# Optimization experiments

Hardware: AMD Instinct MI355X
Metric: run time of the kernel (lower is better)

## Reference

```python
import jax, jax.numpy as jnp
import numpy as np

IN_CH = 32
OUT_CH = 32
HIDDEN = 32  # edge/angle MLP hidden width


def setup_inputs() -> dict:
    key = jax.random.key(0)
    ks = jax.random.split(key, 13)
    N, E, A = 50000, 200000, 400000
    s = 0.1
    return {
        "x": jax.random.normal(ks[0], (N, IN_CH), dtype=jnp.float32),
        "edge_index": jax.random.randint(ks[1], (2, E), 0, N),
        "edge_attr": jax.random.uniform(ks[2], (E, 1), dtype=jnp.float32),
        "angle_index": jax.random.randint(ks[3], (3, A), 0, N),
        "angles": jax.random.uniform(ks[4], (A, 1), dtype=jnp.float32),
        # edge_mlp: Linear(1,32) -> ReLU -> Linear(32, in*out)
        "eW1": jax.random.normal(ks[5], (1, HIDDEN), dtype=jnp.float32) * s,
        "eb1": jax.random.normal(ks[6], (HIDDEN,), dtype=jnp.float32) * s,
        "eW2": jax.random.normal(ks[7], (HIDDEN, IN_CH * OUT_CH), dtype=jnp.float32) * s,
        "eb2": jax.random.normal(ks[8], (IN_CH * OUT_CH,), dtype=jnp.float32) * s,
        # angle_mlp: Linear(1,32) -> ReLU -> Linear(32, out)
        "aW1": jax.random.normal(ks[9], (1, HIDDEN), dtype=jnp.float32) * s,
        "ab1": jax.random.normal(ks[10], (HIDDEN,), dtype=jnp.float32) * s,
        "aW2": jax.random.normal(ks[11], (HIDDEN, OUT_CH), dtype=jnp.float32) * s,
        "ab2": jax.random.normal(ks[12], (OUT_CH,), dtype=jnp.float32) * s,
    }


def reference(x, edge_index, edge_attr, angle_index, angles,
              eW1, eb1, eW2, eb2, aW1, ab1, aW2, ab2):
    N = x.shape[0]
    row, col = edge_index[0], edge_index[1]
    # per-edge weight matrices from edge MLP: (E, in, out)
    h = jax.nn.relu(edge_attr @ eW1 + eb1)
    edge_w = (h @ eW2 + eb2).reshape(-1, IN_CH, OUT_CH)
    # gather source node features, apply per-edge matrix (bmm)
    msg = jnp.einsum('ei,eio->eo', x[col], edge_w)  # (E, out)
    agg = jax.ops.segment_sum(msg, row, num_segments=N)
    # angle branch: scatter angle features onto center node j
    j = angle_index[1]
    angle_feat = jax.nn.relu(angles @ aW1 + ab1) @ aW2 + ab2  # (A, out)
    agg = agg + jax.ops.segment_sum(angle_feat, j, num_segments=N)
    return agg
```

## Files before the change

### kernel.cpp

```cpp
#include <hip/hip_runtime.h>
#include <hip/hip_bf16.h>
#include <stdint.h>

#define IC 32
#define OC 32
#define HID 32

#define PBIN 16
#define TSH 44
#define TSCALE 1048576.0f

typedef __attribute__((ext_vector_type(8))) _Float16 half8;
typedef __attribute__((ext_vector_type(4))) float f32x4;
typedef unsigned long long u64;

static __device__ __forceinline__ _Float16 f2h(float f) { return (_Float16)f; }

__global__ void zero_kernel(float* __restrict__ out, int n) {
    int i = (blockIdx.x * blockDim.x + threadIdx.x) * 4;
    if (i + 3 < n) {
        *(float4*)(out + i) = make_float4(0.f, 0.f, 0.f, 0.f);
    } else {
        for (int k = i; k < n; ++k) out[k] = 0.f;
    }
}

__global__ __launch_bounds__(256) void angle_scatter(
    const float* __restrict__ angles, const int* __restrict__ angle_index,
    const float* __restrict__ aW1, const float* __restrict__ ab1,
    u64* __restrict__ cells, int A)
{
    float w1[HID], b1[HID];
#pragma unroll
    for (int k = 0; k < HID; ++k) { w1[k] = aW1[k]; b1[k] = ab1[k]; }

    int i0 = blockIdx.x * blockDim.x + threadIdx.x;
    int stride = gridDim.x * blockDim.x;
    for (int a = i0; a < A; a += stride) {
        const float t = angles[a];
        const int j = angle_index[A + a];
        int c = 0, c0 = 0;
#pragma unroll
        for (int k = 0; k < HID; ++k) {
            const bool pos = w1[k] > 0.f;
            const bool on  = fmaf(t, w1[k], b1[k]) > 0.f;
            const bool on0 = b1[k] > 0.f;
            c  += (pos ? on  : !on ) ? 1 : 0;
            c0 += (pos ? on0 : !on0) ? 1 : 0;
        }
        const int cc = c - c0;
        if ((unsigned)cc < (unsigned)PBIN) {
            const u64 enc = ((u64)1 << TSH) | (u64)(unsigned)(t * TSCALE);
            atomicAdd(cells + (size_t)j * PBIN + cc, enc);
        }
    }
}

__global__ __launch_bounds__(256) void angle_gather(
    float* __restrict__ out,
    const float* __restrict__ aW1, const float* __restrict__ ab1,
    const float* __restrict__ aW2, const float* __restrict__ ab2,
    int N)
{
    const int lane = threadIdx.x & 63;
    const int o    = lane & 31;
    const int half = lane >> 5;
    const int wib  = threadIdx.x >> 6;
    const int gw   = blockIdx.x * (blockDim.x >> 6) + wib;
    const int nodesPerIter = gridDim.x * (blockDim.x >> 6) * 2;

    float w1[HID], b1[HID], w2[HID];
#pragma unroll
    for (int k = 0; k < HID; ++k) {
        w1[k] = aW1[k];
        b1[k] = ab1[k];
        w2[k] = aW2[k * OC + o];
    }
    const float bias = ab2[o];

    for (int j = gw * 2 + half; j < N; j += nodesPerIter) {
        const u64* cj = (const u64*)out + (size_t)j * PBIN;
        float acc = 0.f, tot = 0.f;
#pragma unroll
        for (int cc = 0; cc < PBIN; ++cc) {
            const u64 v = cj[cc];
            if (v) {
                const float n  = (float)(unsigned)(v >> TSH);
                const float ts = (float)(v & (((u64)1 << TSH) - 1)) * (1.f / TSCALE);
                const float tb = ts / n;
                float s = 0.f;
#pragma unroll
                for (int k = 0; k < HID; ++k) {
                    float h = fmaf(tb, w1[k], b1[k]);
                    h = h > 0.f ? h : 0.f;
                    s = fmaf(h, w2[k], s);
                }
                acc = fmaf(n, s, acc);
                tot += n;
            }
        }
        out[(size_t)j * OC + o] = fmaf(tot, bias, acc);
    }
}

__global__ __launch_bounds__(256) void angle_fixup(
    const float* __restrict__ angles, const int* __restrict__ angle_index,
    const float* __restrict__ aW1, const float* __restrict__ ab1,
    const float* __restrict__ aW2, const float* __restrict__ ab2,
    float* __restrict__ out, int A)
{
    float w1[HID], b1[HID];
#pragma unroll
    for (int k = 0; k < HID; ++k) { w1[k] = aW1[k]; b1[k] = ab1[k]; }

    int c0 = 0, c1 = 0;
#pragma unroll
    for (int k = 0; k < HID; ++k) {
        const bool pos = w1[k] > 0.f;
        const bool f0 = pos ? (b1[k] > 0.f) : !(b1[k] > 0.f);
        const bool f1 = pos ? ((w1[k] + b1[k]) > 0.f) : !((w1[k] + b1[k]) > 0.f);
        c0 += f0 ? 1 : 0;
        c1 += f1 ? 1 : 0;
    }
    if (c1 - c0 + 1 <= PBIN) return;

    int i0 = blockIdx.x * blockDim.x + threadIdx.x;
    int stride = gridDim.x * blockDim.x;
    for (int a = i0; a < A; a += stride) {
        const float t = angles[a];
        const int j = angle_index[A + a];
        int c = 0;
#pragma unroll
        for (int k = 0; k < HID; ++k) {
            const bool pos = w1[k] > 0.f;
            const bool on  = fmaf(t, w1[k], b1[k]) > 0.f;
            c += (pos ? on : !on) ? 1 : 0;
        }
        if (c - c0 >= PBIN) {
            float h[HID];
#pragma unroll
            for (int k = 0; k < HID; ++k) {
                float v = fmaf(t, w1[k], b1[k]);
                h[k] = v > 0.f ? v : 0.f;
            }
            for (int o = 0; o < OC; ++o) {
                float s = ab2[o];
#pragma unroll
                for (int k = 0; k < HID; ++k) s = fmaf(h[k], aW2[k * OC + o], s);
                unsafeAtomicAdd(out + (size_t)j * OC + o, s);
            }
        }
    }
}

__global__ __launch_bounds__(256) void edge_kernel(
    const float* __restrict__ x, const int* __restrict__ edge_index,
    const float* __restrict__ edge_attr,
    const float* __restrict__ eW1, const float* __restrict__ eb1,
    const float* __restrict__ eW2, const float* __restrict__ eb2,
    float* __restrict__ out, int E)
{
    const int tid   = threadIdx.x;
    const int lane  = tid & 63;
    const int gwave = blockIdx.x * 4 + (tid >> 6);
    const int ot    = gwave & 1;
    const int tile0 = gwave >> 1;
    const int tstride = (gridDim.x * 4) >> 1;
    const int q     = lane >> 4;
    const int l15   = lane & 15;
    const int ocol  = ot * 16 + l15;

    half8 Bf[33];
#pragma unroll
    for (int s = 0; s < 32; ++s) {
        half8 b;
#pragma unroll
        for (int j = 0; j < 8; ++j)
            b[j] = f2h(eW2[s * 1024 + (q * 8 + j) * 32 + ocol]);
        Bf[s] = b;
    }
    {
        half8 b;
#pragma unroll
        for (int j = 0; j < 8; ++j)
            b[j] = f2h(eb2[(q * 8 + j) * 32 + ocol]);
        Bf[32] = b;
    }

    const int numTiles = (E + 15) >> 4;

    for (int tile = tile0; tile < numTiles; tile += 2 * tstride) {
        const int tA = tile;
        const int tB = tile + tstride;
        const bool hasB = (tB < numTiles);

        const int eA  = (tA << 4) + l15;
        const bool va = (eA < E);
        const int eAc = va ? eA : 0;
        const float ta = va ? edge_attr[eAc] : 0.f;
        const int colA = va ? edge_index[E + eAc] : 0;

        const int eB  = (tB << 4) + l15;
        const bool vb = hasB && (eB < E);
        const int eBc = vb ? eB : 0;
        const float tb = vb ? edge_attr[eBc] : 0.f;
        const int colB = vb ? edge_index[E + eBc] : 0;

        const float* xpA = x + (size_t)colA * IC + q * 8;
        const float4 xloA = *(const float4*)(xpA);
        const float4 xhiA = *(const float4*)(xpA + 4);
        const float* xpB = x + (size_t)colB * IC + q * 8;
        const float4 xloB = *(const float4*)(xpB);
        const float4 xhiB = *(const float4*)(xpB + 4);

        int dstsA[4], dstsB[4];
        const int ebaseA = (tA << 4) + q * 4;
        const int ebaseB = (tB << 4) + q * 4;
#pragma unroll
        for (int r = 0; r < 4; ++r) {
            const int erA = ebaseA + r;
            dstsA[r] = (erA < E) ? edge_index[erA] : -1;
            const int erB = ebaseB + r;
            dstsB[r] = (hasB && erB < E) ? edge_index[erB] : -1;
        }

        half8 xhA, xhB;
        xhA[0] = f2h(xloA.x); xhA[1] = f2h(xloA.y);
        xhA[2] = f2h(xloA.z); xhA[3] = f2h(xloA.w);
        xhA[4] = f2h(xhiA.x); xhA[5] = f2h(xhiA.y);
        xhA[6] = f2h(xhiA.z); xhA[7] = f2h(xhiA.w);
        xhB[0] = f2h(xloB.x); xhB[1] = f2h(xloB.y);
        xhB[2] = f2h(xloB.z); xhB[3] = f2h(xloB.w);
        xhB[4] = f2h(xhiB.x); xhB[5] = f2h(xhiB.y);
        xhB[6] = f2h(xhiB.z); xhB[7] = f2h(xhiB.w);

        f32x4 accA = {0.f, 0.f, 0.f, 0.f};
        f32x4 accB = {0.f, 0.f, 0.f, 0.f};
#pragma unroll
        for (int s = 0; s < 32; ++s) {
            const float w1s = eW1[s], b1s = eb1[s];
            float hsA = fmaf(ta, w1s, b1s);
            hsA = hsA > 0.f ? hsA : 0.f;
            float hsB = fmaf(tb, w1s, b1s);
            hsB = hsB > 0.f ? hsB : 0.f;
            const _Float16 hA = f2h(hsA);
            const _Float16 hB = f2h(hsB);
            half8 hvA = {hA, hA, hA, hA, hA, hA, hA, hA};
            half8 hvB = {hB, hB, hB, hB, hB, hB, hB, hB};
            half8 aA = xhA * hvA;
            half8 aB = xhB * hvB;
            accA = __builtin_amdgcn_mfma_f32_16x16x32_f16(aA, Bf[s], accA, 0, 0, 0);
            accB = __builtin_amdgcn_mfma_f32_16x16x32_f16(aB, Bf[s], accB, 0, 0, 0);
        }
        {
            accA = __builtin_amdgcn_mfma_f32_16x16x32_f16(xhA, Bf[32], accA, 0, 0, 0);
            accB = __builtin_amdgcn_mfma_f32_16x16x32_f16(xhB, Bf[32], accB, 0, 0, 0);
        }

#pragma unroll
        for (int r = 0; r < 4; ++r) {
            if (dstsA[r] >= 0)
                unsafeAtomicAdd(out + (size_t)dstsA[r] * OC + ocol, accA[r]);
        }
#pragma unroll
        for (int r = 0; r < 4; ++r) {
            if (dstsB[r] >= 0)
                unsafeAtomicAdd(out + (size_t)dstsB[r] * OC + ocol, accB[r]);
        }
    }
}

extern "C" void kernel_launch(void* const* d_in, const int* in_sizes, int n_in,
                              void* d_out, int out_size, void* d_ws, size_t ws_size,
                              hipStream_t stream)
{
    const float* x          = (const float*)d_in[0];
    const int*   edge_index = (const int*)d_in[1];
    const float* edge_attr  = (const float*)d_in[2];
    const int*   angle_index= (const int*)d_in[3];
    const float* angles     = (const float*)d_in[4];
    const float* eW1        = (const float*)d_in[5];
    const float* eb1        = (const float*)d_in[6];
    const float* eW2        = (const float*)d_in[7];
    const float* eb2        = (const float*)d_in[8];
    const float* aW1        = (const float*)d_in[9];
    const float* ab1        = (const float*)d_in[10];
    const float* aW2        = (const float*)d_in[11];
    const float* ab2        = (const float*)d_in[12];
    float* out = (float*)d_out;
    (void)d_ws; (void)ws_size;

    const int E = in_sizes[1] / 2;
    const int A = in_sizes[3] / 3;
    const int N = in_sizes[0] / IC;

    const int zblocks = (out_size / 4 + 255) / 256;
    zero_kernel<<<zblocks, 256, 0, stream>>>(out, out_size);

    const int sblocks = (A + 255) / 256;
    angle_scatter<<<sblocks, 256, 0, stream>>>(angles, angle_index,
                                               aW1, ab1, (u64*)out, A);

    const int gblocks = (N + 7) / 8;
    angle_gather<<<gblocks, 256, 0, stream>>>(out, aW1, ab1, aW2, ab2, N);

    angle_fixup<<<sblocks, 256, 0, stream>>>(angles, angle_index,
                                             aW1, ab1, aW2, ab2, out, A);

    edge_kernel<<<512, 256, 0, stream>>>(x, edge_index, edge_attr,
                                         eW1, eb1, eW2, eb2, out, E);
}
```

Measured before the change: 191.9 us.

## Rewrite angle_gather to accumulate hidden activations and apply aW2 via MFMA

The angle gather kernel now sums per-cell hidden activations, weighted by cell count, for 16 nodes per wave, with each quarter-wave handling 8 of the 32 hidden units. It then applies the second layer with two fp16 16x16x32 MFMA instructions instead of a per-output scalar dot product for every cell. It also limits the loop over cells to the number of possible ReLU pieces computed from the weights, rather than always walking all 16 bins. This removes most of the redundant scalar FMAs and bin reads, but rounds the accumulated activations and aW2 to fp16, which may cost accuracy.

```diff
diff --git a/kernel.cpp b/kernel.cpp
--- a/kernel.cpp
+++ b/kernel.cpp
@@ -63,43 +63,73 @@
     int N)
 {
     const int lane = threadIdx.x & 63;
-    const int o    = lane & 31;
-    const int half = lane >> 5;
+    const int q    = lane >> 4;
+    const int l15  = lane & 15;
     const int wib  = threadIdx.x >> 6;
-    const int gw   = blockIdx.x * (blockDim.x >> 6) + wib;
-    const int nodesPerIter = gridDim.x * (blockDim.x >> 6) * 2;
-
-    float w1[HID], b1[HID], w2[HID];
+    const int base = (blockIdx.x * 4 + wib) * 16;
+    if (base >= N) return;
+
+    float w1s[8], b1s[8];
+    int c0 = 0, c1 = 0;
 #pragma unroll
     for (int k = 0; k < HID; ++k) {
-        w1[k] = aW1[k];
-        b1[k] = ab1[k];
-        w2[k] = aW2[k * OC + o];
-    }
-    const float bias = ab2[o];
-
-    for (int j = gw * 2 + half; j < N; j += nodesPerIter) {
-        const u64* cj = (const u64*)out + (size_t)j * PBIN;
-        float acc = 0.f, tot = 0.f;
-#pragma unroll
-        for (int cc = 0; cc < PBIN; ++cc) {
-            const u64 v = cj[cc];
-            if (v) {
-                const float n  = (float)(unsigned)(v >> TSH);
-                const float ts = (float)(v & (((u64)1 << TSH) - 1)) * (1.f / TSCALE);
-                const float tb = ts / n;
-                float s = 0.f;
-#pragma unroll
-                for (int k = 0; k < HID; ++k) {
-                    float h = fmaf(tb, w1[k], b1[k]);
-                    h = h > 0.f ? h : 0.f;
-                    s = fmaf(h, w2[k], s);
-                }
-                acc = fmaf(n, s, acc);
-                tot += n;
+        const float w = aW1[k], b = ab1[k];
+        const bool pos = w > 0.f;
+        const bool f0 = pos ? (b > 0.f) : !(b > 0.f);
+        const bool f1 = pos ? ((w + b) > 0.f) : !((w + b) > 0.f);
+        c0 += f0 ? 1 : 0;
+        c1 += f1 ? 1 : 0;
+        if ((k >> 3) == q) { w1s[k & 7] = w; b1s[k & 7] = b; }
+    }
+    int npc = c1 - c0 + 1;
+    if (npc > PBIN) npc = PBIN;
+
+    half8 Bf0, Bf1;
+#pragma unroll
+    for (int j = 0; j < 8; ++j) {
+        Bf0[j] = f2h(aW2[(q * 8 + j) * OC + l15]);
+        Bf1[j] = f2h(aW2[(q * 8 + j) * OC + 16 + l15]);
+    }
+    const float bias0 = ab2[l15];
+    const float bias1 = ab2[16 + l15];
+
+    const int jn = base + l15;
+    const bool vn = (jn < N);
+    const u64* cj = (const u64*)out + (size_t)(vn ? jn : 0) * PBIN;
+    float g[8] = {0.f, 0.f, 0.f, 0.f, 0.f, 0.f, 0.f, 0.f};
+    float tot = 0.f;
+    for (int cc = 0; cc < npc; ++cc) {
+        const u64 v = vn ? cj[cc] : 0;
+        if (v) {
+            const float n  = (float)(unsigned)(v >> TSH);
+            const float ts = (float)(v & (((u64)1 << TSH) - 1)) * (1.f / TSCALE);
+            const float tb = ts / n;
+#pragma unroll
+            for (int k = 0; k < 8; ++k) {
+                float h = fmaf(tb, w1s[k], b1s[k]);
+                h = h > 0.f ? h : 0.f;
+                g[k] = fmaf(n, h, g[k]);
             }
-        }
-        out[(size_t)j * OC + o] = fmaf(tot, bias, acc);
+            tot += n;
+        }
+    }
+    half8 a;
+#pragma unroll
+    for (int k = 0; k < 8; ++k) a[k] = f2h(g[k]);
+
+    f32x4 acc0 = {0.f, 0.f, 0.f, 0.f};
+    f32x4 acc1 = {0.f, 0.f, 0.f, 0.f};
+    acc0 = __builtin_amdgcn_mfma_f32_16x16x32_f16(a, Bf0, acc0, 0, 0, 0);
+    acc1 = __builtin_amdgcn_mfma_f32_16x16x32_f16(a, Bf1, acc1, 0, 0, 0);
+
+#pragma unroll
+    for (int r = 0; r < 4; ++r) {
+        const int node = base + q * 4 + r;
+        const float tr = __shfl(tot, q * 4 + r, 64);
+        if (node < N) {
+            out[(size_t)node * OC + l15]      = fmaf(tr, bias0, acc0[r]);
+            out[(size_t)node * OC + 16 + l15] = fmaf(tr, bias1, acc1[r]);
+        }
     }
 }
 
@@ -301,7 +331,7 @@
     angle_scatter<<<sblocks, 256, 0, stream>>>(angles, angle_index,
                                                aW1, ab1, (u64*)out, A);
 
-    const int gblocks = (N + 7) / 8;
+    const int gblocks = (N + 63) / 64;
     angle_gather<<<gblocks, 256, 0, stream>>>(out, aW1, ab1, aW2, ab2, N);
 
     angle_fixup<<<sblocks, 256, 0, stream>>>(angles, angle_index,
```

Result: faster. 166.8 us (-13.1%).
